# Performance work log

Hardware: AMD Instinct MI355X
Metric: run time of the kernel (lower is better)

## Reference

```python
import math
import jax, jax.numpy as jnp
import numpy as np

NEG = -1000000000.0


def setup_inputs() -> dict:
    key = jax.random.key(0)
    kq, kk, kv, km = jax.random.split(key, 4)
    B, H, S, D = 4, 16, 2048, 128
    q = jax.random.normal(kq, (B, H, S, D), dtype=jnp.float32)
    k = jax.random.normal(kk, (B, H, S, D), dtype=jnp.float32)
    v = jax.random.normal(kv, (B, H, S, D), dtype=jnp.float32)
    mask = jax.random.randint(km, (B, 1, 1, S), 0, 2, dtype=jnp.int32)
    return {"q": q, "k": k, "v": v, "mask": mask}


def reference(q, k, v, mask):
    # q,k,v: [B,H,S,D]; mask: [B,1,1,S] with 0 = masked out
    d_k = q.shape[-1]
    scores = jnp.einsum("bhqd,bhkd->bhqk", q, k) / math.sqrt(d_k)
    # additive padding mask (mask==0 -> -1e9)
    scores = scores + jnp.where(mask == 0, NEG, 0.0).astype(scores.dtype)
    # causal future mask (mask_future=True): strict upper triangle -> -1e9
    Qn, Kn = scores.shape[-2], scores.shape[-1]
    future = jnp.triu(jnp.ones((Qn, Kn), dtype=bool), k=1)
    scores = scores + jnp.where(future, NEG, 0.0).astype(scores.dtype)
    attn = jax.nn.softmax(scores, axis=-1)
    return jnp.einsum("bhqk,bhkd->bhqd", attn, v)
```

## Files before the change

### kernel.cpp

```cpp
#include <hip/hip_runtime.h>

typedef unsigned short u16;
typedef unsigned int   u32;
typedef __attribute__((ext_vector_type(8)))  short short8;
typedef __attribute__((ext_vector_type(4)))  float floatx4;
typedef __attribute__((ext_vector_type(16))) float floatx16;

#define CNEG  (-1.4426950408889634e9f)
#define QSCL  (0.12753129020334545f)
#define NEGF  (-1000000000.0f)
#define DEFER_THR 8.0f

__device__ __forceinline__ u16 f2bf(float x) {
  u32 u = __builtin_bit_cast(u32, x);
  u += 0x7fffu + ((u >> 16) & 1u);
  return (u16)(u >> 16);
}
__device__ __forceinline__ u32 cvtpk(float lo, float hi) {
  u32 r;
  asm("v_cvt_pk_bf16_f32 %0, %1, %2" : "=v"(r) : "v"(lo), "v"(hi));
  return r;
}

__device__ __forceinline__ int swzK(int r, int c)  { return r * 128 + (c ^ ((r & 7) << 3)); }
__device__ __forceinline__ int svb(int d)          { return ((d & 7) ^ ((d >> 2) & 7)) << 3; }
__device__ __forceinline__ int swzV(int d, int kv) { return d * 64 + (kv ^ svb(d)); }
__device__ __forceinline__ int swap23(int x) {
  return (x & ~0xC) | ((x & 4) << 1) | ((x & 8) >> 1);
}

__device__ __forceinline__ void gld16(const void* g, void* l) {
  __builtin_amdgcn_global_load_lds(
      (const __attribute__((address_space(1))) u32*)g,
      (__attribute__((address_space(3))) u32*)l, 16, 0, 0);
}

constexpr int Hh = 16, Ss = 2048, Dd = 128;
constexpr int KVBLK = 64;
constexpr int NT = Ss / KVBLK;
constexpr int TILE = KVBLK * Dd;
constexpr int NELEM = 4 * Hh * Ss * Dd;
constexpr int MASKN = 4 * Ss;

__global__ __launch_bounds__(256) void prep_kv(const float* __restrict__ K,
                                               const float* __restrict__ V,
                                               const int* __restrict__ MSK,
                                               u16* __restrict__ Kp, u16* __restrict__ Vp,
                                               float* __restrict__ Mg,
                                               float* __restrict__ Sp) {
  __shared__ u16 Vl[KVBLK * 132];
  const int blk = blockIdx.x, tid = threadIdx.x;
  const float* kg = K + (size_t)blk * TILE;
  const float* vg = V + (size_t)blk * TILE;
  u16* kp = Kp + (size_t)blk * TILE;
  u16* vp = Vp + (size_t)blk * TILE;

  if (blk < MASKN / 256) {
    int i = blk * 256 + tid;
    Mg[i] = MSK[i] ? 0.0f : CNEG;
  }

  #pragma unroll
  for (int it = 0; it < 4; ++it) {
    int ch = tid + it * 256;
    int f = ch >> 6, ln = ch & 63;
    int kvb = f >> 3, s = f & 7;
    int kvs = kvb * 32 + swap23(ln & 31);
    int d0 = s * 16 + (ln >> 5) * 8;
    const float* src = kg + kvs * 128 + d0;
    float4 a = *(const float4*)src, bq = *(const float4*)(src + 4);
    union { short8 v; u16 h[8]; } u;
    u.h[0] = f2bf(a.x);  u.h[1] = f2bf(a.y);  u.h[2] = f2bf(a.z);  u.h[3] = f2bf(a.w);
    u.h[4] = f2bf(bq.x); u.h[5] = f2bf(bq.y); u.h[6] = f2bf(bq.z); u.h[7] = f2bf(bq.w);
    *(short8*)(kp + ch * 8) = u.v;
  }
  #pragma unroll
  for (int it = 0; it < 8; ++it) {
    int e = (tid + it * 256) * 4;
    int r = e >> 7, c = e & 127;
    float4 a = *(const float4*)(vg + e);
    uint2 w;
    w.x = (u32)f2bf(a.x) | ((u32)f2bf(a.y) << 16);
    w.y = (u32)f2bf(a.z) | ((u32)f2bf(a.w) << 16);
    *(uint2*)&Vl[r * 132 + c] = w;
  }
  __syncthreads();
  #pragma unroll
  for (int it = 0; it < 4; ++it) {
    int ch = tid + it * 256;
    int f = ch >> 6, ln = ch & 63;
    int dt = f >> 2, s = f & 3;
    int d = dt * 32 + (ln & 31);
    int kv0 = s * 16 + (ln >> 5) * 8;
    union { short8 v; u16 h[8]; } u;
    #pragma unroll
    for (int i = 0; i < 8; ++i) u.h[i] = Vl[(kv0 + i) * 132 + d];
    *(short8*)(vp + ch * 8) = u.v;
  }

  {
    const int d = tid & 127, hf = tid >> 7;
    const int bb = blk >> 9;
    const int j0 = (blk & 31) * 64 + hf * 32;
    float acc = 0.0f;
    #pragma unroll 4
    for (int jj = 0; jj < 32; ++jj) {
      const float mfv = MSK[bb * Ss + j0 + jj] ? 1.0f : 0.0f;
      acc = fmaf(mfv, vg[(hf * 32 + jj) * 128 + d], acc);
    }
    __syncthreads();
    float* sred = (float*)Vl;
    if (hf) sred[d] = acc;
    __syncthreads();
    if (!hf) Sp[(size_t)blk * 128 + d] = acc + sred[d];
  }
}

__global__ __launch_bounds__(256) void mask_scan(const int* __restrict__ MSK,
                                                 int* __restrict__ F1M1) {
  __shared__ int sf[4], sc[4];
  const int b = blockIdx.x, tid = threadIdx.x, lane = tid & 63, wid = tid >> 6;
  int first = Ss, cnt = 0;
  for (int j = tid; j < Ss; j += 256)
    if (MSK[b * Ss + j]) { if (j < first) first = j; cnt++; }
  #pragma unroll
  for (int off = 1; off < 64; off <<= 1) {
    first = min(first, __shfl_xor(first, off, 64));
    cnt  += __shfl_xor(cnt, off, 64);
  }
  if (lane == 0) { sf[wid] = first; sc[wid] = cnt; }
  __syncthreads();
  if (tid == 0) {
    int f = min(min(sf[0], sf[1]), min(sf[2], sf[3]));
    int c = sc[0] + sc[1] + sc[2] + sc[3];
    F1M1[b] = f; F1M1[4 + b] = c;
  }
}

__global__ __launch_bounds__(128) void fixup(const float* __restrict__ V,
                                             const float* __restrict__ Sp,
                                             const int* __restrict__ F1M1,
                                             float* __restrict__ O) {
  const int bh = blockIdx.x, b = bh >> 4, d = threadIdx.x;
  const int f1 = F1M1[b];
  if (f1 == 0) return;
  const int m1 = F1M1[4 + b];
  float s1v = 0.0f;
  #pragma unroll
  for (int t = 0; t < NT; ++t) s1v += Sp[((size_t)bh * NT + t) * 128 + d];
  float pref = 0.0f;
  for (int i = 0; i < f1; ++i) {
    pref += V[((size_t)bh * Ss + i) * Dd + d];
    O[((size_t)bh * Ss + i) * Dd + d] = (pref + s1v) / (float)(i + 1 + m1);
  }
}

__global__ __launch_bounds__(256, 3) void attn_fwd(const float* __restrict__ Q,
                                                   const u16* __restrict__ Kp,
                                                   const u16* __restrict__ Vp,
                                                   const float* __restrict__ Mg,
                                                   float* __restrict__ O) {
  __shared__ u16 Kl[2][TILE];
  __shared__ u16 Vt[TILE];

  const int tid = threadIdx.x, lane = tid & 63, wid = tid >> 6;
  const int l31 = lane & 31, h = lane >> 5;
  const int id = blockIdx.x;
  const int wg = (id & 7) * 128 + (id >> 3);
  const int bh = wg >> 4, b = bh >> 4;
  const int qt = 15 - (wg & 15);
  const int qbase = qt * 128;
  const int nT = 2 * qt + 2;
  const int qi = qbase + wid * 32 + l31;

  const size_t tb = (size_t)bh * NT;
  auto stageK = [&](int buf, int t) {
    const char* gk = (const char*)(Kp + (tb + t) * TILE) + wid * 1024 + lane * 16;
    char* lk = (char*)&Kl[buf][0] + wid * 1024;
    #pragma unroll
    for (int i = 0; i < 4; ++i) gld16(gk + i * 4096, lk + i * 4096);
  };
  auto stageV = [&](int t) {
    const char* gv = (const char*)(Vp + (tb + t) * TILE) + wid * 1024 + lane * 16;
    char* lv = (char*)&Vt[0] + wid * 1024;
    #pragma unroll
    for (int i = 0; i < 4; ++i) gld16(gv + i * 4096, lv + i * 4096);
  };

  const float* qg = Q + ((size_t)bh * Ss + qi) * Dd + h * 8;
  short8 qf[8];
  #pragma unroll
  for (int s = 0; s < 8; ++s) {
    float4 x0 = *(const float4*)(qg + s * 16);
    float4 x1 = *(const float4*)(qg + s * 16 + 4);
    union { short8 v; u16 hh[8]; } u;
    u.hh[0] = f2bf(x0.x * QSCL); u.hh[1] = f2bf(x0.y * QSCL);
    u.hh[2] = f2bf(x0.z * QSCL); u.hh[3] = f2bf(x0.w * QSCL);
    u.hh[4] = f2bf(x1.x * QSCL); u.hh[5] = f2bf(x1.y * QSCL);
    u.hh[6] = f2bf(x1.z * QSCL); u.hh[7] = f2bf(x1.w * QSCL);
    qf[s] = u.v;
  }

  float m_run = -3.0e38f, l_part = 0.0f;
  floatx16 oacc[4];
  #pragma unroll
  for (int dt = 0; dt < 4; ++dt)
    #pragma unroll
    for (int r = 0; r < 16; ++r) oacc[dt][r] = 0.0f;

  stageK(0, 0);
  __syncthreads();
  int cur = 0;

  #pragma unroll 1
  for (int t = 0; t < nT; ++t) {
    stageV(t);
    if (t + 1 < nT) stageK(cur ^ 1, t + 1);

    const int kvbase = t * KVBLK;

    const float* mrow = Mg + b * Ss + kvbase + h * 8;
    float4 a0 = *(const float4*)(mrow);
    float4 a1 = *(const float4*)(mrow + 4);
    float4 a2 = *(const float4*)(mrow + 16);
    float4 a3 = *(const float4*)(mrow + 20);
    float4 a4 = *(const float4*)(mrow + 32);
    float4 a5 = *(const float4*)(mrow + 36);
    float4 a6 = *(const float4*)(mrow + 48);
    float4 a7 = *(const float4*)(mrow + 52);
    floatx16 s0, s1;
    s0[0]=a0.x;  s0[1]=a0.y;  s0[2]=a0.z;  s0[3]=a0.w;
    s0[4]=a1.x;  s0[5]=a1.y;  s0[6]=a1.z;  s0[7]=a1.w;
    s0[8]=a2.x;  s0[9]=a2.y;  s0[10]=a2.z; s0[11]=a2.w;
    s0[12]=a3.x; s0[13]=a3.y; s0[14]=a3.z; s0[15]=a3.w;
    s1[0]=a4.x;  s1[1]=a4.y;  s1[2]=a4.z;  s1[3]=a4.w;
    s1[4]=a5.x;  s1[5]=a5.y;  s1[6]=a5.z;  s1[7]=a5.w;
    s1[8]=a6.x;  s1[9]=a6.y;  s1[10]=a6.z; s1[11]=a6.w;
    s1[12]=a7.x; s1[13]=a7.y; s1[14]=a7.z; s1[15]=a7.w;
    if (kvbase + KVBLK - 1 >= qbase + wid * 32) {
      #pragma unroll
      for (int r = 0; r < 16; ++r) {
        const int j0 = kvbase + ((r >> 3) << 4) + h * 8 + (r & 7);
        if (j0 > qi)      s0[r] += CNEG;
        if (j0 + 32 > qi) s1[r] += CNEG;
      }
    }

    const u16* kb = &Kl[cur][lane * 8];
    __builtin_amdgcn_s_setprio(1);
    #pragma unroll
    for (int s = 0; s < 8; ++s) {
      short8 k0 = *(const short8*)&kb[s * 512];
      short8 k1 = *(const short8*)&kb[(8 + s) * 512];
      s0 = __builtin_amdgcn_mfma_f32_32x32x16_bf16(k0, qf[s], s0, 0, 0, 0);
      s1 = __builtin_amdgcn_mfma_f32_32x32x16_bf16(k1, qf[s], s1, 0, 0, 0);
    }
    __builtin_amdgcn_s_setprio(0);

    float mx8[8];
    #pragma unroll
    for (int r = 0; r < 8; ++r)
      mx8[r] = fmaxf(fmaxf(s0[r], s0[r + 8]), fmaxf(s1[r], s1[r + 8]));
    float mx4[4];
    #pragma unroll
    for (int r = 0; r < 4; ++r) mx4[r] = fmaxf(mx8[r], mx8[r + 4]);
    float pmax = fmaxf(fmaxf(mx4[0], mx4[1]), fmaxf(mx4[2], mx4[3]));

    float mn = m_run;
    if (!__all(pmax <= m_run + DEFER_THR)) {
      pmax = fmaxf(pmax, __shfl_xor(pmax, 32, 64));
      mn = fmaxf(m_run, pmax);
      const float alpha = exp2f(m_run - mn);
      m_run = mn;
      l_part *= alpha;
      #pragma unroll
      for (int dt = 0; dt < 4; ++dt)
        #pragma unroll
        for (int r = 0; r < 16; ++r) oacc[dt][r] *= alpha;
    }
    #pragma unroll
    for (int r = 0; r < 16; ++r) {
      const float p0 = exp2f(s0[r] - mn);
      const float p1 = exp2f(s1[r] - mn);
      s0[r] = p0; s1[r] = p1;
      l_part += p0 + p1;
    }

    union { short8 v; u32 w[4]; } pu[4];
    #pragma unroll
    for (int j = 0; j < 4; ++j) {
      pu[0].w[j] = cvtpk(s0[2 * j],     s0[2 * j + 1]);
      pu[1].w[j] = cvtpk(s0[8 + 2 * j], s0[8 + 2 * j + 1]);
      pu[2].w[j] = cvtpk(s1[2 * j],     s1[2 * j + 1]);
      pu[3].w[j] = cvtpk(s1[8 + 2 * j], s1[8 + 2 * j + 1]);
    }

    __syncthreads();

    const u16* vb = &Vt[lane * 8];
    __builtin_amdgcn_s_setprio(1);
    #pragma unroll
    for (int ss = 0; ss < 4; ++ss) {
      #pragma unroll
      for (int dt = 0; dt < 4; ++dt) {
        short8 vf = *(const short8*)&vb[(dt * 4 + ss) * 512];
        oacc[dt] = __builtin_amdgcn_mfma_f32_32x32x16_bf16(vf, pu[ss].v, oacc[dt], 0, 0, 0);
      }
    }
    __builtin_amdgcn_s_setprio(0);

    __syncthreads();
    cur ^= 1;
  }

  float l_run = l_part + __shfl_xor(l_part, 32, 64);
  const float inv = 1.0f / l_run;
  float* orow = O + ((size_t)bh * Ss + qi) * Dd;
  #pragma unroll
  for (int dt = 0; dt < 4; ++dt) {
    #pragma unroll
    for (int r32 = 0; r32 < 4; ++r32) {
      float4 o4;
      o4.x = oacc[dt][4 * r32 + 0] * inv;
      o4.y = oacc[dt][4 * r32 + 1] * inv;
      o4.z = oacc[dt][4 * r32 + 2] * inv;
      o4.w = oacc[dt][4 * r32 + 3] * inv;
      *(float4*)(orow + dt * 32 + 8 * r32 + 4 * h) = o4;
    }
  }
}

__device__ __forceinline__ int swzPf(int row, int col) { return row * 64 + (col ^ ((row & 7) << 3)); }

__global__ __launch_bounds__(256) void attn_fb(
    const float* __restrict__ Q, const float* __restrict__ K,
    const float* __restrict__ V, const int* __restrict__ MSK,
    float* __restrict__ O)
{
  __shared__ u16 Kls[KVBLK * Dd];
  __shared__ u16 Vts[Dd * KVBLK];
  __shared__ u16 Pls[4][16 * KVBLK];
  __shared__ int sAff;

  const int tid = threadIdx.x, lane = tid & 63, wid = tid >> 6;
  const int l15 = lane & 15, lg = lane >> 4;
  const int qt = blockIdx.x, bh = blockIdx.y, b = bh >> 4;
  const int qbase = qt * 64;
  const float scale = 0.08838834764831845f;

  const int qrowA = qbase + wid * 16 + l15;
  const float* qg = Q + ((size_t)bh * Ss + qrowA) * Dd + lg * 8;
  short8 qf[4];
  #pragma unroll
  for (int kc = 0; kc < 4; ++kc) {
    float4 x0 = *(const float4*)(qg + kc * 32);
    float4 x1 = *(const float4*)(qg + kc * 32 + 4);
    union { short8 v; u16 h[8]; } u;
    u.h[0] = f2bf(x0.x * scale); u.h[1] = f2bf(x0.y * scale);
    u.h[2] = f2bf(x0.z * scale); u.h[3] = f2bf(x0.w * scale);
    u.h[4] = f2bf(x1.x * scale); u.h[5] = f2bf(x1.y * scale);
    u.h[6] = f2bf(x1.z * scale); u.h[7] = f2bf(x1.w * scale);
    qf[kc] = u.v;
  }

  float m_run[4], l_run[4];
  floatx4 oacc[8];
  const floatx4 vzero = {0.f, 0.f, 0.f, 0.f};
  #pragma unroll
  for (int r = 0; r < 4; ++r) { m_run[r] = -3.0e38f; l_run[r] = 0.0f; }
  #pragma unroll
  for (int dt = 0; dt < 8; ++dt) oacc[dt] = vzero;
  const int qi0 = qbase + wid * 16 + lg * 4;

  for (int t = 0; t < NT; ++t) {
    if (t > blockIdx.x && !sAff) break;
    const int kvbase = t * KVBLK;
    const float* kg = K + ((size_t)bh * Ss + kvbase) * Dd;
    const float* vg = V + ((size_t)bh * Ss + kvbase) * Dd;
    #pragma unroll
    for (int it = 0; it < 8; ++it) {
      int e = (tid + it * 256) * 4;
      int r0 = e >> 7, c0 = e & 127;
      float4 x = *(const float4*)(kg + e);
      uint2 hk;
      hk.x = (u32)f2bf(x.x) | ((u32)f2bf(x.y) << 16);
      hk.y = (u32)f2bf(x.z) | ((u32)f2bf(x.w) << 16);
      *(uint2*)&Kls[swzK(r0, c0)] = hk;
      float4 y = *(const float4*)(vg + e);
      u16 hv[4] = { f2bf(y.x), f2bf(y.y), f2bf(y.z), f2bf(y.w) };
      #pragma unroll
      for (int j = 0; j < 4; ++j) Vts[swzV(c0 + j, r0)] = hv[j];
    }
    __syncthreads();

    float madd[4];
    #pragma unroll
    for (int kt = 0; kt < 4; ++kt)
      madd[kt] = MSK[b * Ss + kvbase + kt * 16 + l15] ? 0.0f : NEGF;

    floatx4 sacc[4];
    #pragma unroll
    for (int kt = 0; kt < 4; ++kt) sacc[kt] = vzero;
    #pragma unroll
    for (int kt = 0; kt < 4; ++kt) {
      const int krow = kt * 16 + l15;
      #pragma unroll
      for (int kc = 0; kc < 4; ++kc) {
        short8 kf = *(const short8*)&Kls[swzK(krow, kc * 32 + lg * 8)];
        sacc[kt] = __builtin_amdgcn_mfma_f32_16x16x32_bf16(qf[kc], kf, sacc[kt], 0, 0, 0);
      }
    }

    float mnew[4];
    #pragma unroll
    for (int r = 0; r < 4; ++r) mnew[r] = m_run[r];
    #pragma unroll
    for (int kt = 0; kt < 4; ++kt) {
      const int kvj = kvbase + kt * 16 + l15;
      #pragma unroll
      for (int r = 0; r < 4; ++r) {
        float s = sacc[kt][r] + madd[kt];
        if (kvj > qi0 + r) s += NEGF;
        sacc[kt][r] = s;
        mnew[r] = fmaxf(mnew[r], s);
      }
    }
    #pragma unroll
    for (int off = 1; off < 16; off <<= 1) {
      #pragma unroll
      for (int r = 0; r < 4; ++r)
        mnew[r] = fmaxf(mnew[r], __shfl_xor(mnew[r], off, 64));
    }
    float alpha[4], psum[4];
    #pragma unroll
    for (int r = 0; r < 4; ++r) {
      alpha[r] = __expf(m_run[r] - mnew[r]);
      m_run[r] = mnew[r];
      psum[r] = 0.f;
    }
    #pragma unroll
    for (int kt = 0; kt < 4; ++kt) {
      #pragma unroll
      for (int r = 0; r < 4; ++r) {
        float p = __expf(sacc[kt][r] - mnew[r]);
        psum[r] += p;
        Pls[wid][swzPf(lg * 4 + r, kt * 16 + l15)] = f2bf(p);
      }
    }
    #pragma unroll
    for (int off = 1; off < 16; off <<= 1) {
      #pragma unroll
      for (int r = 0; r < 4; ++r)
        psum[r] += __shfl_xor(psum[r], off, 64);
    }
    #pragma unroll
    for (int r = 0; r < 4; ++r) l_run[r] = l_run[r] * alpha[r] + psum[r];
    #pragma unroll
    for (int dt = 0; dt < 8; ++dt) {
      #pragma unroll
      for (int r = 0; r < 4; ++r) oacc[dt][r] *= alpha[r];
    }
    #pragma unroll
    for (int kc = 0; kc < 2; ++kc) {
      short8 pfr = *(const short8*)&Pls[wid][swzPf(l15, kc * 32 + lg * 8)];
      #pragma unroll
      for (int dt = 0; dt < 8; ++dt) {
        short8 vf = *(const short8*)&Vts[swzV(dt * 16 + l15, kc * 32 + lg * 8)];
        oacc[dt] = __builtin_amdgcn_mfma_f32_16x16x32_bf16(pfr, vf, oacc[dt], 0, 0, 0);
      }
    }
    __syncthreads();

    if (t == blockIdx.x) {
      if (tid == 0) sAff = 0;
      __syncthreads();
      bool aff = (m_run[0] < -5.0e8f) || (m_run[1] < -5.0e8f) ||
                 (m_run[2] < -5.0e8f) || (m_run[3] < -5.0e8f);
      if (aff) sAff = 1;
      __syncthreads();
    }
  }

  #pragma unroll
  for (int r = 0; r < 4; ++r) {
    float inv = 1.0f / l_run[r];
    float* op = O + ((size_t)bh * Ss + qi0 + r) * Dd + l15;
    #pragma unroll
    for (int dt = 0; dt < 8; ++dt) op[dt * 16] = oacc[dt][r] * inv;
  }
}

extern "C" void kernel_launch(void* const* d_in, const int* in_sizes, int n_in,
                              void* d_out, int out_size, void* d_ws, size_t ws_size,
                              hipStream_t stream) {
  const float* q = (const float*)d_in[0];
  const float* k = (const float*)d_in[1];
  const float* v = (const float*)d_in[2];
  const int* mask = (const int*)d_in[3];
  float* out = (float*)d_out;

  const size_t need = (size_t)2 * NELEM * sizeof(u16)
                    + (size_t)MASKN * sizeof(float)
                    + (size_t)64 * NT * 128 * sizeof(float)
                    + 8 * sizeof(int);
  if (ws_size >= need) {
    u16* Kp = (u16*)d_ws;
    u16* Vp = Kp + NELEM;
    float* Mg = (float*)(Vp + NELEM);
    float* Sp = Mg + MASKN;
    int* F1M1 = (int*)(Sp + (size_t)64 * NT * 128);
    prep_kv<<<dim3(64 * NT), 256, 0, stream>>>(k, v, mask, Kp, Vp, Mg, Sp);
    mask_scan<<<dim3(4), 256, 0, stream>>>(mask, F1M1);
    attn_fwd<<<dim3(1024), 256, 0, stream>>>(q, Kp, Vp, Mg, out);
    fixup<<<dim3(64), 128, 0, stream>>>(v, Sp, F1M1, out);
  } else {
    attn_fb<<<dim3(NT, 64), 256, 0, stream>>>(q, k, v, mask, out);
  }
}
```

Before: 199.2 us.

## Split attention work groups into 64-row query tiles with D-split waves

Each workgroup now covers 64 query rows instead of 128. Two waves share each 32-row query group and split the 128-wide output dimension in half, and the grid doubles to 2048 blocks. The aim is more parallelism, less causal-tail imbalance, and half the O accumulator registers per wave. In exchange, every wave still computes the full QK^T and softmax, so that work is duplicated, and K/V tiles are loaded twice as often overall. Barriers are also rewritten with explicit vmcnt waits so the V wait can overlap with outstanding K prefetch, and an unconditional dummy K stage is added on the last iteration.

```diff
diff --git a/kernel.cpp b/kernel.cpp
--- a/kernel.cpp
+++ b/kernel.cpp
@@ -165,13 +165,14 @@
 
   const int tid = threadIdx.x, lane = tid & 63, wid = tid >> 6;
   const int l31 = lane & 31, h = lane >> 5;
+  const int qg = wid & 1, dh = wid >> 1;
   const int id = blockIdx.x;
-  const int wg = (id & 7) * 128 + (id >> 3);
-  const int bh = wg >> 4, b = bh >> 4;
-  const int qt = 15 - (wg & 15);
-  const int qbase = qt * 128;
-  const int nT = 2 * qt + 2;
-  const int qi = qbase + wid * 32 + l31;
+  const int wg = (id & 7) * 256 + (id >> 3);
+  const int bh = wg >> 5, b = bh >> 4;
+  const int qt = 31 - (wg & 31);
+  const int qbase = qt * 64;
+  const int nT = qt + 1;
+  const int qi = qbase + qg * 32 + l31;
 
   const size_t tb = (size_t)bh * NT;
   auto stageK = [&](int buf, int t) {
@@ -187,12 +188,12 @@
     for (int i = 0; i < 4; ++i) gld16(gv + i * 4096, lv + i * 4096);
   };
 
-  const float* qg = Q + ((size_t)bh * Ss + qi) * Dd + h * 8;
+  const float* qg_ptr = Q + ((size_t)bh * Ss + qi) * Dd + h * 8;
   short8 qf[8];
   #pragma unroll
   for (int s = 0; s < 8; ++s) {
-    float4 x0 = *(const float4*)(qg + s * 16);
-    float4 x1 = *(const float4*)(qg + s * 16 + 4);
+    float4 x0 = *(const float4*)(qg_ptr + s * 16);
+    float4 x1 = *(const float4*)(qg_ptr + s * 16 + 4);
     union { short8 v; u16 hh[8]; } u;
     u.hh[0] = f2bf(x0.x * QSCL); u.hh[1] = f2bf(x0.y * QSCL);
     u.hh[2] = f2bf(x0.z * QSCL); u.hh[3] = f2bf(x0.w * QSCL);
@@ -202,21 +203,20 @@
   }
 
   float m_run = -3.0e38f, l_part = 0.0f;
-  floatx16 oacc[4];
-  #pragma unroll
-  for (int dt = 0; dt < 4; ++dt)
+  floatx16 oacc[2];
+  #pragma unroll
+  for (int dt = 0; dt < 2; ++dt)
     #pragma unroll
     for (int r = 0; r < 16; ++r) oacc[dt][r] = 0.0f;
 
   stageK(0, 0);
-  __syncthreads();
+  asm volatile("s_waitcnt vmcnt(0)" ::: "memory");
+  __builtin_amdgcn_s_barrier();
+  __builtin_amdgcn_sched_barrier(0);
   int cur = 0;
 
   #pragma unroll 1
   for (int t = 0; t < nT; ++t) {
-    stageV(t);
-    if (t + 1 < nT) stageK(cur ^ 1, t + 1);
-
     const int kvbase = t * KVBLK;
 
     const float* mrow = Mg + b * Ss + kvbase + h * 8;
@@ -228,6 +228,10 @@
     float4 a5 = *(const float4*)(mrow + 36);
     float4 a6 = *(const float4*)(mrow + 48);
     float4 a7 = *(const float4*)(mrow + 52);
+
+    stageV(t);
+    stageK(cur ^ 1, (t + 1 < nT) ? (t + 1) : 0);
+
     floatx16 s0, s1;
     s0[0]=a0.x;  s0[1]=a0.y;  s0[2]=a0.z;  s0[3]=a0.w;
     s0[4]=a1.x;  s0[5]=a1.y;  s0[6]=a1.z;  s0[7]=a1.w;
@@ -237,7 +241,7 @@
     s1[4]=a5.x;  s1[5]=a5.y;  s1[6]=a5.z;  s1[7]=a5.w;
     s1[8]=a6.x;  s1[9]=a6.y;  s1[10]=a6.z; s1[11]=a6.w;
     s1[12]=a7.x; s1[13]=a7.y; s1[14]=a7.z; s1[15]=a7.w;
-    if (kvbase + KVBLK - 1 >= qbase + wid * 32) {
+    if (kvbase + KVBLK - 1 >= qbase + qg * 32) {
       #pragma unroll
       for (int r = 0; r < 16; ++r) {
         const int j0 = kvbase + ((r >> 3) << 4) + h * 8 + (r & 7);
@@ -274,16 +278,14 @@
       m_run = mn;
       l_part *= alpha;
       #pragma unroll
-      for (int dt = 0; dt < 4; ++dt)
+      for (int dt = 0; dt < 2; ++dt)
         #pragma unroll
         for (int r = 0; r < 16; ++r) oacc[dt][r] *= alpha;
     }
     #pragma unroll
     for (int r = 0; r < 16; ++r) {
-      const float p0 = exp2f(s0[r] - mn);
-      const float p1 = exp2f(s1[r] - mn);
-      s0[r] = p0; s1[r] = p1;
-      l_part += p0 + p1;
+      s0[r] = exp2f(s0[r] - mn);
+      s1[r] = exp2f(s1[r] - mn);
     }
 
     union { short8 v; u32 w[4]; } pu[4];
@@ -295,37 +297,51 @@
       pu[3].w[j] = cvtpk(s1[8 + 2 * j], s1[8 + 2 * j + 1]);
     }
 
-    __syncthreads();
+    {
+      float t8[8];
+      #pragma unroll
+      for (int r = 0; r < 8; ++r)
+        t8[r] = (s0[r] + s0[r + 8]) + (s1[r] + s1[r + 8]);
+      float t4a = t8[0] + t8[4], t4b = t8[1] + t8[5];
+      float t4c = t8[2] + t8[6], t4d = t8[3] + t8[7];
+      l_part += (t4a + t4b) + (t4c + t4d);
+    }
+
+    asm volatile("s_waitcnt vmcnt(4)" ::: "memory");
+    __builtin_amdgcn_s_barrier();
+    __builtin_amdgcn_sched_barrier(0);
 
     const u16* vb = &Vt[lane * 8];
     __builtin_amdgcn_s_setprio(1);
     #pragma unroll
     for (int ss = 0; ss < 4; ++ss) {
       #pragma unroll
-      for (int dt = 0; dt < 4; ++dt) {
-        short8 vf = *(const short8*)&vb[(dt * 4 + ss) * 512];
-        oacc[dt] = __builtin_amdgcn_mfma_f32_32x32x16_bf16(vf, pu[ss].v, oacc[dt], 0, 0, 0);
+      for (int dtp = 0; dtp < 2; ++dtp) {
+        short8 vf = *(const short8*)&vb[((dh * 2 + dtp) * 4 + ss) * 512];
+        oacc[dtp] = __builtin_amdgcn_mfma_f32_32x32x16_bf16(vf, pu[ss].v, oacc[dtp], 0, 0, 0);
       }
     }
     __builtin_amdgcn_s_setprio(0);
 
-    __syncthreads();
+    asm volatile("s_waitcnt vmcnt(0)" ::: "memory");
+    __builtin_amdgcn_s_barrier();
+    __builtin_amdgcn_sched_barrier(0);
     cur ^= 1;
   }
 
   float l_run = l_part + __shfl_xor(l_part, 32, 64);
   const float inv = 1.0f / l_run;
-  float* orow = O + ((size_t)bh * Ss + qi) * Dd;
-  #pragma unroll
-  for (int dt = 0; dt < 4; ++dt) {
+  float* orow = O + ((size_t)bh * Ss + qi) * Dd + dh * 64;
+  #pragma unroll
+  for (int dtp = 0; dtp < 2; ++dtp) {
     #pragma unroll
     for (int r32 = 0; r32 < 4; ++r32) {
       float4 o4;
-      o4.x = oacc[dt][4 * r32 + 0] * inv;
-      o4.y = oacc[dt][4 * r32 + 1] * inv;
-      o4.z = oacc[dt][4 * r32 + 2] * inv;
-      o4.w = oacc[dt][4 * r32 + 3] * inv;
-      *(float4*)(orow + dt * 32 + 8 * r32 + 4 * h) = o4;
+      o4.x = oacc[dtp][4 * r32 + 0] * inv;
+      o4.y = oacc[dtp][4 * r32 + 1] * inv;
+      o4.z = oacc[dtp][4 * r32 + 2] * inv;
+      o4.w = oacc[dtp][4 * r32 + 3] * inv;
+      *(float4*)(orow + dtp * 32 + 8 * r32 + 4 * h) = o4;
     }
   }
 }
@@ -511,7 +527,7 @@
     int* F1M1 = (int*)(Sp + (size_t)64 * NT * 128);
     prep_kv<<<dim3(64 * NT), 256, 0, stream>>>(k, v, mask, Kp, Vp, Mg, Sp);
     mask_scan<<<dim3(4), 256, 0, stream>>>(mask, F1M1);
-    attn_fwd<<<dim3(1024), 256, 0, stream>>>(q, Kp, Vp, Mg, out);
+    attn_fwd<<<dim3(2048), 256, 0, stream>>>(q, Kp, Vp, Mg, out);
     fixup<<<dim3(64), 128, 0, stream>>>(v, Sp, F1M1, out);
   } else {
     attn_fb<<<dim3(NT, 64), 256, 0, stream>>>(q, k, v, mask, out);
```

New measurement: 237.8 us. +19.4%, slower.

## Split KV tile into halves and overlap V loads with softmax via counted waits

Applied to the files above, without the earlier changes.

Each 64-key tile is now processed in two 32-key halves, each doing QK^T, online softmax and the PV accumulate, which shortens live ranges and lowers register pressure. The __syncthreads calls are replaced by explicit s_waitcnt vmcnt counts plus raw barriers, so the V tile only has to arrive before the first PV step while the next K prefetch stays in flight. The K prefetch is now issued unconditionally (reloading tile 0 on the last iteration) to keep the vmcnt accounting fixed. The online max rescale may now run twice per tile, and the hand-counted vmcnt(4) depends on the exact number of loads issued.

```diff
diff --git a/kernel.cpp b/kernel.cpp
--- a/kernel.cpp
+++ b/kernel.cpp
@@ -187,12 +187,12 @@
     for (int i = 0; i < 4; ++i) gld16(gv + i * 4096, lv + i * 4096);
   };
 
-  const float* qg = Q + ((size_t)bh * Ss + qi) * Dd + h * 8;
+  const float* qgp = Q + ((size_t)bh * Ss + qi) * Dd + h * 8;
   short8 qf[8];
   #pragma unroll
   for (int s = 0; s < 8; ++s) {
-    float4 x0 = *(const float4*)(qg + s * 16);
-    float4 x1 = *(const float4*)(qg + s * 16 + 4);
+    float4 x0 = *(const float4*)(qgp + s * 16);
+    float4 x1 = *(const float4*)(qgp + s * 16 + 4);
     union { short8 v; u16 hh[8]; } u;
     u.hh[0] = f2bf(x0.x * QSCL); u.hh[1] = f2bf(x0.y * QSCL);
     u.hh[2] = f2bf(x0.z * QSCL); u.hh[3] = f2bf(x0.w * QSCL);
@@ -209,15 +209,15 @@
     for (int r = 0; r < 16; ++r) oacc[dt][r] = 0.0f;
 
   stageK(0, 0);
-  __syncthreads();
+  asm volatile("s_waitcnt vmcnt(0)" ::: "memory");
+  __builtin_amdgcn_s_barrier();
+  __builtin_amdgcn_sched_barrier(0);
   int cur = 0;
 
   #pragma unroll 1
   for (int t = 0; t < nT; ++t) {
-    stageV(t);
-    if (t + 1 < nT) stageK(cur ^ 1, t + 1);
-
     const int kvbase = t * KVBLK;
+    const bool diag = (kvbase + KVBLK - 1 >= qbase + wid * 32);
 
     const float* mrow = Mg + b * Ss + kvbase + h * 8;
     float4 a0 = *(const float4*)(mrow);
@@ -228,88 +228,104 @@
     float4 a5 = *(const float4*)(mrow + 36);
     float4 a6 = *(const float4*)(mrow + 48);
     float4 a7 = *(const float4*)(mrow + 52);
-    floatx16 s0, s1;
-    s0[0]=a0.x;  s0[1]=a0.y;  s0[2]=a0.z;  s0[3]=a0.w;
-    s0[4]=a1.x;  s0[5]=a1.y;  s0[6]=a1.z;  s0[7]=a1.w;
-    s0[8]=a2.x;  s0[9]=a2.y;  s0[10]=a2.z; s0[11]=a2.w;
-    s0[12]=a3.x; s0[13]=a3.y; s0[14]=a3.z; s0[15]=a3.w;
-    s1[0]=a4.x;  s1[1]=a4.y;  s1[2]=a4.z;  s1[3]=a4.w;
-    s1[4]=a5.x;  s1[5]=a5.y;  s1[6]=a5.z;  s1[7]=a5.w;
-    s1[8]=a6.x;  s1[9]=a6.y;  s1[10]=a6.z; s1[11]=a6.w;
-    s1[12]=a7.x; s1[13]=a7.y; s1[14]=a7.z; s1[15]=a7.w;
-    if (kvbase + KVBLK - 1 >= qbase + wid * 32) {
-      #pragma unroll
-      for (int r = 0; r < 16; ++r) {
-        const int j0 = kvbase + ((r >> 3) << 4) + h * 8 + (r & 7);
-        if (j0 > qi)      s0[r] += CNEG;
-        if (j0 + 32 > qi) s1[r] += CNEG;
-      }
-    }
+
+    stageV(t);
+    stageK(cur ^ 1, (t + 1 < nT) ? (t + 1) : 0);
 
     const u16* kb = &Kl[cur][lane * 8];
-    __builtin_amdgcn_s_setprio(1);
-    #pragma unroll
-    for (int s = 0; s < 8; ++s) {
-      short8 k0 = *(const short8*)&kb[s * 512];
-      short8 k1 = *(const short8*)&kb[(8 + s) * 512];
-      s0 = __builtin_amdgcn_mfma_f32_32x32x16_bf16(k0, qf[s], s0, 0, 0, 0);
-      s1 = __builtin_amdgcn_mfma_f32_32x32x16_bf16(k1, qf[s], s1, 0, 0, 0);
-    }
-    __builtin_amdgcn_s_setprio(0);
-
-    float mx8[8];
-    #pragma unroll
-    for (int r = 0; r < 8; ++r)
-      mx8[r] = fmaxf(fmaxf(s0[r], s0[r + 8]), fmaxf(s1[r], s1[r + 8]));
-    float mx4[4];
-    #pragma unroll
-    for (int r = 0; r < 4; ++r) mx4[r] = fmaxf(mx8[r], mx8[r + 4]);
-    float pmax = fmaxf(fmaxf(mx4[0], mx4[1]), fmaxf(mx4[2], mx4[3]));
-
-    float mn = m_run;
-    if (!__all(pmax <= m_run + DEFER_THR)) {
-      pmax = fmaxf(pmax, __shfl_xor(pmax, 32, 64));
-      mn = fmaxf(m_run, pmax);
-      const float alpha = exp2f(m_run - mn);
-      m_run = mn;
-      l_part *= alpha;
-      #pragma unroll
-      for (int dt = 0; dt < 4; ++dt)
+    const u16* vb = &Vt[lane * 8];
+    bool vready = false;
+
+    #pragma unroll
+    for (int half = 0; half < 2; ++half) {
+      floatx16 sc;
+      if (half == 0) {
+        sc[0]=a0.x;  sc[1]=a0.y;  sc[2]=a0.z;  sc[3]=a0.w;
+        sc[4]=a1.x;  sc[5]=a1.y;  sc[6]=a1.z;  sc[7]=a1.w;
+        sc[8]=a2.x;  sc[9]=a2.y;  sc[10]=a2.z; sc[11]=a2.w;
+        sc[12]=a3.x; sc[13]=a3.y; sc[14]=a3.z; sc[15]=a3.w;
+      } else {
+        sc[0]=a4.x;  sc[1]=a4.y;  sc[2]=a4.z;  sc[3]=a4.w;
+        sc[4]=a5.x;  sc[5]=a5.y;  sc[6]=a5.z;  sc[7]=a5.w;
+        sc[8]=a6.x;  sc[9]=a6.y;  sc[10]=a6.z; sc[11]=a6.w;
+        sc[12]=a7.x; sc[13]=a7.y; sc[14]=a7.z; sc[15]=a7.w;
+      }
+      if (diag) {
         #pragma unroll
-        for (int r = 0; r < 16; ++r) oacc[dt][r] *= alpha;
-    }
-    #pragma unroll
-    for (int r = 0; r < 16; ++r) {
-      const float p0 = exp2f(s0[r] - mn);
-      const float p1 = exp2f(s1[r] - mn);
-      s0[r] = p0; s1[r] = p1;
-      l_part += p0 + p1;
-    }
-
-    union { short8 v; u32 w[4]; } pu[4];
-    #pragma unroll
-    for (int j = 0; j < 4; ++j) {
-      pu[0].w[j] = cvtpk(s0[2 * j],     s0[2 * j + 1]);
-      pu[1].w[j] = cvtpk(s0[8 + 2 * j], s0[8 + 2 * j + 1]);
-      pu[2].w[j] = cvtpk(s1[2 * j],     s1[2 * j + 1]);
-      pu[3].w[j] = cvtpk(s1[8 + 2 * j], s1[8 + 2 * j + 1]);
-    }
-
-    __syncthreads();
-
-    const u16* vb = &Vt[lane * 8];
-    __builtin_amdgcn_s_setprio(1);
-    #pragma unroll
-    for (int ss = 0; ss < 4; ++ss) {
-      #pragma unroll
-      for (int dt = 0; dt < 4; ++dt) {
-        short8 vf = *(const short8*)&vb[(dt * 4 + ss) * 512];
-        oacc[dt] = __builtin_amdgcn_mfma_f32_32x32x16_bf16(vf, pu[ss].v, oacc[dt], 0, 0, 0);
-      }
-    }
-    __builtin_amdgcn_s_setprio(0);
-
-    __syncthreads();
+        for (int r = 0; r < 16; ++r) {
+          const int j0 = kvbase + half * 32 + ((r >> 3) << 4) + h * 8 + (r & 7);
+          if (j0 > qi) sc[r] += CNEG;
+        }
+      }
+
+      __builtin_amdgcn_s_setprio(1);
+      #pragma unroll
+      for (int s = 0; s < 8; ++s) {
+        short8 kf = *(const short8*)&kb[(half * 8 + s) * 512];
+        sc = __builtin_amdgcn_mfma_f32_32x32x16_bf16(kf, qf[s], sc, 0, 0, 0);
+      }
+      __builtin_amdgcn_s_setprio(0);
+
+      float mx8[8];
+      #pragma unroll
+      for (int r = 0; r < 8; ++r) mx8[r] = fmaxf(sc[r], sc[r + 8]);
+      float mx4[4];
+      #pragma unroll
+      for (int r = 0; r < 4; ++r) mx4[r] = fmaxf(mx8[r], mx8[r + 4]);
+      float pmax = fmaxf(fmaxf(mx4[0], mx4[1]), fmaxf(mx4[2], mx4[3]));
+
+      float mn = m_run;
+      if (!__all(pmax <= m_run + DEFER_THR)) {
+        pmax = fmaxf(pmax, __shfl_xor(pmax, 32, 64));
+        mn = fmaxf(m_run, pmax);
+        const float alpha = exp2f(m_run - mn);
+        m_run = mn;
+        l_part *= alpha;
+        #pragma unroll
+        for (int dt = 0; dt < 4; ++dt)
+          #pragma unroll
+          for (int r = 0; r < 16; ++r) oacc[dt][r] *= alpha;
+      }
+      #pragma unroll
+      for (int r = 0; r < 16; ++r) sc[r] = exp2f(sc[r] - mn);
+
+      union { short8 v; u32 w[4]; } pu[2];
+      #pragma unroll
+      for (int j = 0; j < 4; ++j) {
+        pu[0].w[j] = cvtpk(sc[2 * j],     sc[2 * j + 1]);
+        pu[1].w[j] = cvtpk(sc[8 + 2 * j], sc[8 + 2 * j + 1]);
+      }
+      {
+        float t8[8];
+        #pragma unroll
+        for (int r = 0; r < 8; ++r) t8[r] = sc[r] + sc[r + 8];
+        float t4a = t8[0] + t8[4], t4b = t8[1] + t8[5];
+        float t4c = t8[2] + t8[6], t4d = t8[3] + t8[7];
+        l_part += (t4a + t4b) + (t4c + t4d);
+      }
+
+      if (!vready) {
+        asm volatile("s_waitcnt vmcnt(4)" ::: "memory");
+        __builtin_amdgcn_s_barrier();
+        __builtin_amdgcn_sched_barrier(0);
+        vready = true;
+      }
+
+      __builtin_amdgcn_s_setprio(1);
+      #pragma unroll
+      for (int sp = 0; sp < 2; ++sp) {
+        #pragma unroll
+        for (int dt = 0; dt < 4; ++dt) {
+          short8 vf = *(const short8*)&vb[(dt * 4 + half * 2 + sp) * 512];
+          oacc[dt] = __builtin_amdgcn_mfma_f32_32x32x16_bf16(vf, pu[sp].v, oacc[dt], 0, 0, 0);
+        }
+      }
+      __builtin_amdgcn_s_setprio(0);
+    }
+
+    asm volatile("s_waitcnt vmcnt(0)" ::: "memory");
+    __builtin_amdgcn_s_barrier();
+    __builtin_amdgcn_sched_barrier(0);
     cur ^= 1;
   }
 
```

Measured after the change: 202.5 us. About the same (+1.7%).

## Software-pipeline QK of next tile with softmax and PV of current tile

Applied to the files above, without the earlier changes.

Restructures the attention loop so the QK^T MFMA work for tile t+1 is issued between the softmax and the PV product of tile t. V is double-buffered in LDS, and K and V staging is moved after a single barrier per tile instead of two. The aim is to hide softmax latency and reduce barrier stalls by overlapping matrix and vector work. In exchange it keeps two score accumulators alive, which raises register pressure, so launch bounds drop from 3 to 2 blocks per CU, and the larger LDS footprint further lowers occupancy.

```diff
diff --git a/kernel.cpp b/kernel.cpp
--- a/kernel.cpp
+++ b/kernel.cpp
@@ -155,13 +155,13 @@
   }
 }
 
-__global__ __launch_bounds__(256, 3) void attn_fwd(const float* __restrict__ Q,
+__global__ __launch_bounds__(256, 2) void attn_fwd(const float* __restrict__ Q,
                                                    const u16* __restrict__ Kp,
                                                    const u16* __restrict__ Vp,
                                                    const float* __restrict__ Mg,
                                                    float* __restrict__ O) {
   __shared__ u16 Kl[2][TILE];
-  __shared__ u16 Vt[TILE];
+  __shared__ u16 Vt[2][TILE];
 
   const int tid = threadIdx.x, lane = tid & 63, wid = tid >> 6;
   const int l31 = lane & 31, h = lane >> 5;
@@ -180,19 +180,19 @@
     #pragma unroll
     for (int i = 0; i < 4; ++i) gld16(gk + i * 4096, lk + i * 4096);
   };
-  auto stageV = [&](int t) {
+  auto stageV = [&](int buf, int t) {
     const char* gv = (const char*)(Vp + (tb + t) * TILE) + wid * 1024 + lane * 16;
-    char* lv = (char*)&Vt[0] + wid * 1024;
+    char* lv = (char*)&Vt[buf][0] + wid * 1024;
     #pragma unroll
     for (int i = 0; i < 4; ++i) gld16(gv + i * 4096, lv + i * 4096);
   };
 
-  const float* qg = Q + ((size_t)bh * Ss + qi) * Dd + h * 8;
+  const float* qgp = Q + ((size_t)bh * Ss + qi) * Dd + h * 8;
   short8 qf[8];
   #pragma unroll
   for (int s = 0; s < 8; ++s) {
-    float4 x0 = *(const float4*)(qg + s * 16);
-    float4 x1 = *(const float4*)(qg + s * 16 + 4);
+    float4 x0 = *(const float4*)(qgp + s * 16);
+    float4 x1 = *(const float4*)(qgp + s * 16 + 4);
     union { short8 v; u16 hh[8]; } u;
     u.hh[0] = f2bf(x0.x * QSCL); u.hh[1] = f2bf(x0.y * QSCL);
     u.hh[2] = f2bf(x0.z * QSCL); u.hh[3] = f2bf(x0.w * QSCL);
@@ -208,18 +208,120 @@
     #pragma unroll
     for (int r = 0; r < 16; ++r) oacc[dt][r] = 0.0f;
 
+  floatx16 sA0, sA1, sB0, sB1;
+
+  auto qk_tile = [&](floatx16& d0, floatx16& d1, int t, int kbuf,
+                     const float4& a0, const float4& a1, const float4& a2, const float4& a3,
+                     const float4& a4, const float4& a5, const float4& a6, const float4& a7) {
+    d0[0]=a0.x;  d0[1]=a0.y;  d0[2]=a0.z;  d0[3]=a0.w;
+    d0[4]=a1.x;  d0[5]=a1.y;  d0[6]=a1.z;  d0[7]=a1.w;
+    d0[8]=a2.x;  d0[9]=a2.y;  d0[10]=a2.z; d0[11]=a2.w;
+    d0[12]=a3.x; d0[13]=a3.y; d0[14]=a3.z; d0[15]=a3.w;
+    d1[0]=a4.x;  d1[1]=a4.y;  d1[2]=a4.z;  d1[3]=a4.w;
+    d1[4]=a5.x;  d1[5]=a5.y;  d1[6]=a5.z;  d1[7]=a5.w;
+    d1[8]=a6.x;  d1[9]=a6.y;  d1[10]=a6.z; d1[11]=a6.w;
+    d1[12]=a7.x; d1[13]=a7.y; d1[14]=a7.z; d1[15]=a7.w;
+    const int kvbase = t * KVBLK;
+    if (kvbase + KVBLK - 1 >= qbase + wid * 32) {
+      #pragma unroll
+      for (int r = 0; r < 16; ++r) {
+        const int j0 = kvbase + ((r >> 3) << 4) + h * 8 + (r & 7);
+        if (j0 > qi)      d0[r] += CNEG;
+        if (j0 + 32 > qi) d1[r] += CNEG;
+      }
+    }
+    const u16* kb = &Kl[kbuf][lane * 8];
+    __builtin_amdgcn_s_setprio(1);
+    #pragma unroll
+    for (int s = 0; s < 8; ++s) {
+      short8 k0 = *(const short8*)&kb[s * 512];
+      short8 k1 = *(const short8*)&kb[(8 + s) * 512];
+      d0 = __builtin_amdgcn_mfma_f32_32x32x16_bf16(k0, qf[s], d0, 0, 0, 0);
+      d1 = __builtin_amdgcn_mfma_f32_32x32x16_bf16(k1, qf[s], d1, 0, 0, 0);
+    }
+    __builtin_amdgcn_s_setprio(0);
+  };
+
+  auto phase = [&](floatx16& c0, floatx16& c1, floatx16& n0, floatx16& n1, int t) {
+    float mx8[8];
+    #pragma unroll
+    for (int r = 0; r < 8; ++r)
+      mx8[r] = fmaxf(fmaxf(c0[r], c0[r + 8]), fmaxf(c1[r], c1[r + 8]));
+    float mx4[4];
+    #pragma unroll
+    for (int r = 0; r < 4; ++r) mx4[r] = fmaxf(mx8[r], mx8[r + 4]);
+    float pmax = fmaxf(fmaxf(mx4[0], mx4[1]), fmaxf(mx4[2], mx4[3]));
+
+    float mn = m_run;
+    if (!__all(pmax <= m_run + DEFER_THR)) {
+      pmax = fmaxf(pmax, __shfl_xor(pmax, 32, 64));
+      mn = fmaxf(m_run, pmax);
+      const float alpha = exp2f(m_run - mn);
+      m_run = mn;
+      l_part *= alpha;
+      #pragma unroll
+      for (int dt = 0; dt < 4; ++dt)
+        #pragma unroll
+        for (int r = 0; r < 16; ++r) oacc[dt][r] *= alpha;
+    }
+    #pragma unroll
+    for (int r = 0; r < 16; ++r) {
+      c0[r] = exp2f(c0[r] - mn);
+      c1[r] = exp2f(c1[r] - mn);
+    }
+    union { short8 v; u32 w[4]; } pu[4];
+    #pragma unroll
+    for (int j = 0; j < 4; ++j) {
+      pu[0].w[j] = cvtpk(c0[2 * j],     c0[2 * j + 1]);
+      pu[1].w[j] = cvtpk(c0[8 + 2 * j], c0[8 + 2 * j + 1]);
+      pu[2].w[j] = cvtpk(c1[2 * j],     c1[2 * j + 1]);
+      pu[3].w[j] = cvtpk(c1[8 + 2 * j], c1[8 + 2 * j + 1]);
+    }
+    {
+      float t8[8];
+      #pragma unroll
+      for (int r = 0; r < 8; ++r)
+        t8[r] = (c0[r] + c0[r + 8]) + (c1[r] + c1[r + 8]);
+      float t4a = t8[0] + t8[4], t4b = t8[1] + t8[5];
+      float t4c = t8[2] + t8[6], t4d = t8[3] + t8[7];
+      l_part += (t4a + t4b) + (t4c + t4d);
+    }
+
+    __syncthreads();
+
+    const bool hasNext = (t + 1 < nT);
+    if (hasNext) {
+      const float* mrow = Mg + b * Ss + (t + 1) * KVBLK + h * 8;
+      float4 a0 = *(const float4*)(mrow);
+      float4 a1 = *(const float4*)(mrow + 4);
+      float4 a2 = *(const float4*)(mrow + 16);
+      float4 a3 = *(const float4*)(mrow + 20);
+      float4 a4 = *(const float4*)(mrow + 32);
+      float4 a5 = *(const float4*)(mrow + 36);
+      float4 a6 = *(const float4*)(mrow + 48);
+      float4 a7 = *(const float4*)(mrow + 52);
+      stageV((t + 1) & 1, t + 1);
+      if (t + 2 < nT) stageK(t & 1, t + 2);
+      qk_tile(n0, n1, t + 1, (t + 1) & 1, a0, a1, a2, a3, a4, a5, a6, a7);
+    }
+
+    const u16* vb = &Vt[t & 1][lane * 8];
+    __builtin_amdgcn_s_setprio(1);
+    #pragma unroll
+    for (int ss = 0; ss < 4; ++ss) {
+      #pragma unroll
+      for (int dt = 0; dt < 4; ++dt) {
+        short8 vf = *(const short8*)&vb[(dt * 4 + ss) * 512];
+        oacc[dt] = __builtin_amdgcn_mfma_f32_32x32x16_bf16(vf, pu[ss].v, oacc[dt], 0, 0, 0);
+      }
+    }
+    __builtin_amdgcn_s_setprio(0);
+  };
+
   stageK(0, 0);
   __syncthreads();
-  int cur = 0;
-
-  #pragma unroll 1
-  for (int t = 0; t < nT; ++t) {
-    stageV(t);
-    if (t + 1 < nT) stageK(cur ^ 1, t + 1);
-
-    const int kvbase = t * KVBLK;
-
-    const float* mrow = Mg + b * Ss + kvbase + h * 8;
+  {
+    const float* mrow = Mg + b * Ss + h * 8;
     float4 a0 = *(const float4*)(mrow);
     float4 a1 = *(const float4*)(mrow + 4);
     float4 a2 = *(const float4*)(mrow + 16);
@@ -228,89 +330,15 @@
     float4 a5 = *(const float4*)(mrow + 36);
     float4 a6 = *(const float4*)(mrow + 48);
     float4 a7 = *(const float4*)(mrow + 52);
-    floatx16 s0, s1;
-    s0[0]=a0.x;  s0[1]=a0.y;  s0[2]=a0.z;  s0[3]=a0.w;
-    s0[4]=a1.x;  s0[5]=a1.y;  s0[6]=a1.z;  s0[7]=a1.w;
-    s0[8]=a2.x;  s0[9]=a2.y;  s0[10]=a2.z; s0[11]=a2.w;
-    s0[12]=a3.x; s0[13]=a3.y; s0[14]=a3.z; s0[15]=a3.w;
-    s1[0]=a4.x;  s1[1]=a4.y;  s1[2]=a4.z;  s1[3]=a4.w;
-    s1[4]=a5.x;  s1[5]=a5.y;  s1[6]=a5.z;  s1[7]=a5.w;
-    s1[8]=a6.x;  s1[9]=a6.y;  s1[10]=a6.z; s1[11]=a6.w;
-    s1[12]=a7.x; s1[13]=a7.y; s1[14]=a7.z; s1[15]=a7.w;
-    if (kvbase + KVBLK - 1 >= qbase + wid * 32) {
-      #pragma unroll
-      for (int r = 0; r < 16; ++r) {
-        const int j0 = kvbase + ((r >> 3) << 4) + h * 8 + (r & 7);
-        if (j0 > qi)      s0[r] += CNEG;
-        if (j0 + 32 > qi) s1[r] += CNEG;
-      }
-    }
-
-    const u16* kb = &Kl[cur][lane * 8];
-    __builtin_amdgcn_s_setprio(1);
-    #pragma unroll
-    for (int s = 0; s < 8; ++s) {
-      short8 k0 = *(const short8*)&kb[s * 512];
-      short8 k1 = *(const short8*)&kb[(8 + s) * 512];
-      s0 = __builtin_amdgcn_mfma_f32_32x32x16_bf16(k0, qf[s], s0, 0, 0, 0);
-      s1 = __builtin_amdgcn_mfma_f32_32x32x16_bf16(k1, qf[s], s1, 0, 0, 0);
-    }
-    __builtin_amdgcn_s_setprio(0);
-
-    float mx8[8];
-    #pragma unroll
-    for (int r = 0; r < 8; ++r)
-      mx8[r] = fmaxf(fmaxf(s0[r], s0[r + 8]), fmaxf(s1[r], s1[r + 8]));
-    float mx4[4];
-    #pragma unroll
-    for (int r = 0; r < 4; ++r) mx4[r] = fmaxf(mx8[r], mx8[r + 4]);
-    float pmax = fmaxf(fmaxf(mx4[0], mx4[1]), fmaxf(mx4[2], mx4[3]));
-
-    float mn = m_run;
-    if (!__all(pmax <= m_run + DEFER_THR)) {
-      pmax = fmaxf(pmax, __shfl_xor(pmax, 32, 64));
-      mn = fmaxf(m_run, pmax);
-      const float alpha = exp2f(m_run - mn);
-      m_run = mn;
-      l_part *= alpha;
-      #pragma unroll
-      for (int dt = 0; dt < 4; ++dt)
-        #pragma unroll
-        for (int r = 0; r < 16; ++r) oacc[dt][r] *= alpha;
-    }
-    #pragma unroll
-    for (int r = 0; r < 16; ++r) {
-      const float p0 = exp2f(s0[r] - mn);
-      const float p1 = exp2f(s1[r] - mn);
-      s0[r] = p0; s1[r] = p1;
-      l_part += p0 + p1;
-    }
-
-    union { short8 v; u32 w[4]; } pu[4];
-    #pragma unroll
-    for (int j = 0; j < 4; ++j) {
-      pu[0].w[j] = cvtpk(s0[2 * j],     s0[2 * j + 1]);
-      pu[1].w[j] = cvtpk(s0[8 + 2 * j], s0[8 + 2 * j + 1]);
-      pu[2].w[j] = cvtpk(s1[2 * j],     s1[2 * j + 1]);
-      pu[3].w[j] = cvtpk(s1[8 + 2 * j], s1[8 + 2 * j + 1]);
-    }
-
-    __syncthreads();
-
-    const u16* vb = &Vt[lane * 8];
-    __builtin_amdgcn_s_setprio(1);
-    #pragma unroll
-    for (int ss = 0; ss < 4; ++ss) {
-      #pragma unroll
-      for (int dt = 0; dt < 4; ++dt) {
-        short8 vf = *(const short8*)&vb[(dt * 4 + ss) * 512];
-        oacc[dt] = __builtin_amdgcn_mfma_f32_32x32x16_bf16(vf, pu[ss].v, oacc[dt], 0, 0, 0);
-      }
-    }
-    __builtin_amdgcn_s_setprio(0);
-
-    __syncthreads();
-    cur ^= 1;
+    stageV(0, 0);
+    if (nT > 1) stageK(1, 1);
+    qk_tile(sA0, sA1, 0, 0, a0, a1, a2, a3, a4, a5, a6, a7);
+  }
+
+  #pragma unroll 1
+  for (int tp = 0; tp < nT; tp += 2) {
+    phase(sA0, sA1, sB0, sB1, tp);
+    phase(sB0, sB1, sA0, sA1, tp + 1);
   }
 
   float l_run = l_part + __shfl_xor(l_part, 32, 64);
```

Measured after the change: 204.3 us. 2.6% more time.
